# Kernel optimization log

Measured on AMD Instinct MI355X. Metric: run time of the kernel, lower is better.

Reference implementation:

```python
import jax, jax.numpy as jnp
import numpy as np

B, N, E, H = 32, 512, 256, 8
HD = E // H
EPS = 1e-5

def setup_inputs() -> dict:
    key = jax.random.key(0)
    ks = jax.random.split(key, 10)
    x = jax.random.normal(ks[0], (B, N, E), dtype=jnp.float32)
    # boolean masks: True = masked out. Keep diagonal unmasked so no row is fully masked.
    pre = jax.random.bernoulli(ks[1], 0.1, (B, H, N, N))
    eye = jnp.eye(N, dtype=bool)
    pre_mask = jnp.where(eye[None, None, :, :], False, pre)
    post_attn_mask = jax.random.bernoulli(ks[2], 0.1, (B, N))
    s = 1.0 / np.sqrt(E)
    in_proj_w = jax.random.uniform(ks[3], (3 * E, E), jnp.float32, -s, s)
    in_proj_b = jnp.zeros((3 * E,), jnp.float32)
    out_w = jax.random.uniform(ks[4], (E, E), jnp.float32, -s, s)
    out_b = jnp.zeros((E,), jnp.float32)
    gamma = jnp.ones((E,), jnp.float32)
    beta = jnp.zeros((E,), jnp.float32)
    return {"x": x, "pre_mask": pre_mask, "post_attn_mask": post_attn_mask,
            "in_proj_w": in_proj_w, "in_proj_b": in_proj_b,
            "out_w": out_w, "out_b": out_b, "gamma": gamma, "beta": beta}

def reference(x, pre_mask, post_attn_mask, in_proj_w, in_proj_b, out_w, out_b, gamma, beta):
    b, n, e = x.shape
    # fused qkv projection (matches nn.MultiheadAttention in_proj)
    qkv = x @ in_proj_w.T + in_proj_b            # [B,N,3E]
    q, k, v = jnp.split(qkv, 3, axis=-1)
    def heads(t):
        return t.reshape(b, n, H, HD).transpose(0, 2, 1, 3)  # [B,H,N,HD]
    q, k, v = heads(q), heads(k), heads(v)
    scores = jnp.einsum('bhqd,bhkd->bhqk', q * (HD ** -0.5), k)  # [B,H,N,N]
    scores = jnp.where(pre_mask, -1e9, scores)
    w = jax.nn.softmax(scores, axis=-1)                          # [B,H,N,N]
    o = jnp.einsum('bhqk,bhkd->bhqd', w, v)                      # [B,H,N,HD]
    o = o.transpose(0, 2, 1, 3).reshape(b, n, e)
    o = o @ out_w.T + out_b
    # post-attention mask: zero outputs of unavailable agents
    o = jnp.where(post_attn_mask[:, :, None], 0.0, o)
    # residual + LayerNorm
    y = x + o
    mu = y.mean(axis=-1, keepdims=True)
    var = y.var(axis=-1, keepdims=True)
    out = (y - mu) * jax.lax.rsqrt(var + EPS) * gamma + beta
    # attn_weights averaged over heads (PyTorch default average_attn_weights=True)
    attn_weights = w.mean(axis=1)                                # [B,N,N]
    return (out, attn_weights)
```

## Files before the change

kernel.cpp:

```cpp
#include <hip/hip_runtime.h>

#define BB 32
#define NN 512
#define EE 256
#define HH 8
#define HDD 32

typedef __attribute__((ext_vector_type(4))) float f32x4;
typedef __attribute__((ext_vector_type(8))) short s16x8;
typedef unsigned short ushort_t;
typedef unsigned int uint_t;

__device__ __forceinline__ ushort_t f2bf(float f) {
  union { float f; uint_t u; } v; v.f = f;
  uint_t r = v.u + 0x7fffu + ((v.u >> 16) & 1u);
  return (ushort_t)(r >> 16);
}
__device__ __forceinline__ uint_t pk2(float a, float b) {
  return (uint_t)f2bf(a) | ((uint_t)f2bf(b) << 16);
}
__device__ __forceinline__ float bf2f(ushort_t u) {
  union { uint_t u; float f; } v; v.u = ((uint_t)u) << 16;
  return v.f;
}

__global__ __launch_bounds__(256) void cvt_all(
    const float* __restrict__ x, const float* __restrict__ w1, const float* __restrict__ w2,
    ushort_t* __restrict__ xb, ushort_t* __restrict__ w1b, ushort_t* __restrict__ w2b) {
  const int NX = BB * NN * EE / 4;
  const int NW1 = 3 * EE * EE / 4;
  const int NW2 = EE * EE / 4;
  int i = blockIdx.x * 256 + threadIdx.x;
  const float* src; ushort_t* dst; int j;
  if (i < NX) { src = x; dst = xb; j = i; }
  else if (i < NX + NW1) { src = w1; dst = w1b; j = i - NX; }
  else if (i < NX + NW1 + NW2) { src = w2; dst = w2b; j = i - NX - NW1; }
  else return;
  float4 v = ((const float4*)src)[j];
  uint2 p; p.x = pk2(v.x, v.y); p.y = pk2(v.z, v.w);
  ((uint2*)dst)[j] = p;
}

__global__ __launch_bounds__(256) void qkv_mfma(
    const ushort_t* __restrict__ xb, const ushort_t* __restrict__ wb,
    const float* __restrict__ bias,
    ushort_t* __restrict__ Q, ushort_t* __restrict__ K, ushort_t* __restrict__ Vt) {
  __shared__ ushort_t sA[128][40];
  __shared__ ushort_t sB[128][40];
  int t = threadIdx.x;
  int bj = blockIdx.x % 6, bm = blockIdx.x / 6;
  int m0 = bm * 128, j0 = bj * 128;
  int w4 = t >> 6, lane = t & 63, quad = lane >> 4, l16 = lane & 15;
  int wy = w4 >> 1, wx = w4 & 1;
  f32x4 acc[4][4];
  #pragma unroll
  for (int a = 0; a < 4; a++)
    #pragma unroll
    for (int b = 0; b < 4; b++) acc[a][b] = (f32x4){0.f, 0.f, 0.f, 0.f};
  int sr2 = t >> 2, sc2 = (t & 3) * 8;
  for (int kk = 0; kk < 256; kk += 32) {
    __syncthreads();
    #pragma unroll
    for (int p = 0; p < 2; p++) {
      int r = sr2 + 64 * p;
      *(s16x8*)&sA[r][sc2] = *(const s16x8*)&xb[(size_t)(m0 + r) * 256 + kk + sc2];
      *(s16x8*)&sB[r][sc2] = *(const s16x8*)&wb[(size_t)(j0 + r) * 256 + kk + sc2];
    }
    __syncthreads();
    s16x8 af[4], bf[4];
    #pragma unroll
    for (int mt = 0; mt < 4; mt++)
      af[mt] = *(const s16x8*)&sA[wy * 64 + mt * 16 + l16][quad * 8];
    #pragma unroll
    for (int jt = 0; jt < 4; jt++)
      bf[jt] = *(const s16x8*)&sB[wx * 64 + jt * 16 + l16][quad * 8];
    #pragma unroll
    for (int mt = 0; mt < 4; mt++)
      #pragma unroll
      for (int jt = 0; jt < 4; jt++)
        acc[mt][jt] = __builtin_amdgcn_mfma_f32_16x16x32_bf16(af[mt], bf[jt], acc[mt][jt], 0, 0, 0);
  }
  #pragma unroll
  for (int jt = 0; jt < 4; jt++) {
    int j = j0 + wx * 64 + jt * 16 + l16;
    int which = j >> 8, e0 = j & 255, h = e0 >> 5, d0 = e0 & 31;
    float b = bias[j];
    #pragma unroll
    for (int mt = 0; mt < 4; mt++) {
      #pragma unroll
      for (int r = 0; r < 4; r++) {
        int m = m0 + wy * 64 + mt * 16 + quad * 4 + r;
        int bi = m >> 9, n = m & 511;
        ushort_t val = f2bf(acc[mt][jt][r] + b);
        if (which == 2) {
          Vt[((size_t)(bi * 8 + h) * 32 + d0) * 512 + n] = val;
        } else {
          ushort_t* dst = (which == 0) ? Q : K;
          dst[((size_t)(bi * 8 + h) * 512 + n) * 32 + d0] = val;
        }
      }
    }
  }
}

__global__ __launch_bounds__(256) void attn_fused(
    const ushort_t* __restrict__ Q, const ushort_t* __restrict__ K,
    const ushort_t* __restrict__ Vt, const int* __restrict__ pre_mask,
    const ushort_t* __restrict__ wob, const float* __restrict__ x,
    const float* __restrict__ out_b, const int* __restrict__ post_mask,
    const float* __restrict__ gamma, const float* __restrict__ beta,
    float* __restrict__ out, float* __restrict__ attnw) {
  __shared__ ushort_t sP[4][16 * 132];
  __shared__ float sSum[2][4][16];
  __shared__ float sO[4][16 * 33];
  __shared__ ushort_t sO16[16 * 260];
  __shared__ float sRed1[16][4];
  __shared__ float sRed2[16][4];

  int t = threadIdx.x;
  int bb = blockIdx.x >> 5;
  int q0 = (blockIdx.x & 31) << 4;
  int w = t >> 6, lane = t & 63, quad = lane >> 4, l16 = lane & 15;
  int kbase = w * 128;
  const float scale = 0.17677669529663687f;
  ushort_t* mysP = &sP[w][0];

  float wmean[4][8];
  #pragma unroll
  for (int i = 0; i < 4; i++)
    #pragma unroll
    for (int j = 0; j < 8; j++) wmean[i][j] = 0.f;

  for (int h = 0; h < 8; h++) {
    size_t base = ((size_t)(bb * 8 + h) * 512) * 32;
    const int* mbase = pre_mask + ((size_t)(bb * 8 + h) * 512 + q0) * 512;

    s16x8 afrag = *(const s16x8*)&Q[base + (size_t)(q0 + l16) * 32 + quad * 8];

    float psum[4] = {0.f, 0.f, 0.f, 0.f};
    #pragma unroll
    for (int t8 = 0; t8 < 8; t8++) {
      int n0 = kbase + t8 * 16;
      s16x8 bfrag = *(const s16x8*)&K[base + (size_t)(n0 + l16) * 32 + quad * 8];
      f32x4 acc = {0.f, 0.f, 0.f, 0.f};
      acc = __builtin_amdgcn_mfma_f32_16x16x32_bf16(afrag, bfrag, acc, 0, 0, 0);
      #pragma unroll
      for (int i = 0; i < 4; i++) {
        int msk = mbase[(quad * 4 + i) * 512 + n0 + l16];
        float e = msk ? 0.f : __expf(acc[i] * scale);
        mysP[(quad * 4 + i) * 132 + t8 * 16 + l16] = f2bf(e);
        psum[i] += e;
      }
    }
    #pragma unroll
    for (int i = 0; i < 4; i++) {
      float s = psum[i];
      s += __shfl_xor(s, 1, 64);
      s += __shfl_xor(s, 2, 64);
      s += __shfl_xor(s, 4, 64);
      s += __shfl_xor(s, 8, 64);
      psum[i] = s;
    }
    if (l16 == 0) {
      #pragma unroll
      for (int i = 0; i < 4; i++) sSum[h & 1][w][quad * 4 + i] = psum[i];
    }
    __syncthreads();

    float inv[4];
    #pragma unroll
    for (int i = 0; i < 4; i++) {
      int r = quad * 4 + i;
      inv[i] = 0.125f / (sSum[h & 1][0][r] + sSum[h & 1][1][r] + sSum[h & 1][2][r] + sSum[h & 1][3][r]);
    }
    #pragma unroll
    for (int t8 = 0; t8 < 8; t8++)
      #pragma unroll
      for (int i = 0; i < 4; i++)
        wmean[i][t8] += inv[i] * bf2f(mysP[(quad * 4 + i) * 132 + t8 * 16 + l16]);

    f32x4 oacc[2];
    oacc[0] = (f32x4){0.f, 0.f, 0.f, 0.f};
    oacc[1] = (f32x4){0.f, 0.f, 0.f, 0.f};
    #pragma unroll
    for (int ks = 0; ks < 4; ks++) {
      s16x8 pa = *(const s16x8*)&mysP[l16 * 132 + ks * 32 + quad * 8];
      #pragma unroll
      for (int dt = 0; dt < 2; dt++) {
        s16x8 vb = *(const s16x8*)&Vt[base + (size_t)(dt * 16 + l16) * 512 + kbase + ks * 32 + quad * 8];
        oacc[dt] = __builtin_amdgcn_mfma_f32_16x16x32_bf16(pa, vb, oacc[dt], 0, 0, 0);
      }
    }
    #pragma unroll
    for (int dt = 0; dt < 2; dt++)
      #pragma unroll
      for (int i = 0; i < 4; i++)
        sO[w][(quad * 4 + i) * 33 + dt * 16 + l16] = oacc[dt][i];
    __syncthreads();

    {
      int r = t >> 4;
      int c = (t & 15) * 2;
      float s0 = sO[0][r * 33 + c] + sO[1][r * 33 + c] + sO[2][r * 33 + c] + sO[3][r * 33 + c];
      float s1 = sO[0][r * 33 + c + 1] + sO[1][r * 33 + c + 1] + sO[2][r * 33 + c + 1] + sO[3][r * 33 + c + 1];
      float invr = 1.0f / (sSum[h & 1][0][r] + sSum[h & 1][1][r] + sSum[h & 1][2][r] + sSum[h & 1][3][r]);
      *(uint_t*)&sO16[r * 260 + h * 32 + c] = pk2(s0 * invr, s1 * invr);
    }
  }

  {
    float* arow = attnw + (size_t)(bb * 512 + q0) * 512;
    #pragma unroll
    for (int i = 0; i < 4; i++)
      #pragma unroll
      for (int t8 = 0; t8 < 8; t8++)
        arow[(quad * 4 + i) * 512 + kbase + t8 * 16 + l16] = wmean[i][t8];
  }
  __syncthreads();

  int jr0 = w * 64;
  f32x4 pacc[4];
  #pragma unroll
  for (int jt = 0; jt < 4; jt++) pacc[jt] = (f32x4){0.f, 0.f, 0.f, 0.f};
  #pragma unroll
  for (int kc = 0; kc < 8; kc++) {
    s16x8 pa = *(const s16x8*)&sO16[l16 * 260 + kc * 32 + quad * 8];
    #pragma unroll
    for (int jt = 0; jt < 4; jt++) {
      s16x8 bf = *(const s16x8*)&wob[(size_t)(jr0 + jt * 16 + l16) * 256 + kc * 32 + quad * 8];
      pacc[jt] = __builtin_amdgcn_mfma_f32_16x16x32_bf16(pa, bf, pacc[jt], 0, 0, 0);
    }
  }

  float g4[4], bt4[4], ob4[4];
  #pragma unroll
  for (int jt = 0; jt < 4; jt++) {
    int j = jr0 + jt * 16 + l16;
    g4[jt] = gamma[j]; bt4[jt] = beta[j]; ob4[jt] = out_b[j];
  }
  float yv[4][4];
  #pragma unroll
  for (int i = 0; i < 4; i++) {
    int r = quad * 4 + i;
    int m = bb * 512 + q0 + r;
    bool msk = post_mask[m] != 0;
    float s1 = 0.f, s2 = 0.f;
    #pragma unroll
    for (int jt = 0; jt < 4; jt++) {
      int j = jr0 + jt * 16 + l16;
      float p = msk ? 0.f : (pacc[jt][i] + ob4[jt]);
      float yy = x[(size_t)m * 256 + j] + p;
      yv[i][jt] = yy; s1 += yy; s2 += yy * yy;
    }
    s1 += __shfl_xor(s1, 1, 64); s1 += __shfl_xor(s1, 2, 64);
    s1 += __shfl_xor(s1, 4, 64); s1 += __shfl_xor(s1, 8, 64);
    s2 += __shfl_xor(s2, 1, 64); s2 += __shfl_xor(s2, 2, 64);
    s2 += __shfl_xor(s2, 4, 64); s2 += __shfl_xor(s2, 8, 64);
    if (l16 == 0) { sRed1[r][w] = s1; sRed2[r][w] = s2; }
  }
  __syncthreads();
  #pragma unroll
  for (int i = 0; i < 4; i++) {
    int r = quad * 4 + i;
    int m = bb * 512 + q0 + r;
    float S1 = sRed1[r][0] + sRed1[r][1] + sRed1[r][2] + sRed1[r][3];
    float S2 = sRed2[r][0] + sRed2[r][1] + sRed2[r][2] + sRed2[r][3];
    float mu = S1 * (1.0f / 256.0f);
    float var = S2 * (1.0f / 256.0f) - mu * mu;
    float rstd = rsqrtf(var + 1e-5f);
    #pragma unroll
    for (int jt = 0; jt < 4; jt++) {
      int j = jr0 + jt * 16 + l16;
      out[(size_t)m * 256 + j] = (yv[i][jt] - mu) * rstd * g4[jt] + bt4[jt];
    }
  }
}

extern "C" void kernel_launch(void* const* d_in, const int* in_sizes, int n_in,
                              void* d_out, int out_size, void* d_ws, size_t ws_size,
                              hipStream_t stream) {
  const float* x       = (const float*)d_in[0];
  const int*   pre_m   = (const int*)d_in[1];
  const int*   post_m  = (const int*)d_in[2];
  const float* in_w    = (const float*)d_in[3];
  const float* in_b    = (const float*)d_in[4];
  const float* out_w   = (const float*)d_in[5];
  const float* out_b   = (const float*)d_in[6];
  const float* gamma   = (const float*)d_in[7];
  const float* beta    = (const float*)d_in[8];
  float* out   = (float*)d_out;
  float* attnw = out + (size_t)BB * NN * EE;
  ushort_t* Q   = (ushort_t*)d_ws;
  ushort_t* K   = Q  + (size_t)BB * HH * NN * HDD;
  ushort_t* Vt  = K  + (size_t)BB * HH * NN * HDD;
  ushort_t* xb  = Vt + (size_t)BB * HH * NN * HDD;
  ushort_t* wib = xb + (size_t)BB * NN * EE;
  ushort_t* wob = wib + (size_t)3 * EE * EE;

  const int NCVT = BB * NN * EE / 4 + 3 * EE * EE / 4 + EE * EE / 4;
  cvt_all<<<dim3((NCVT + 255) / 256), dim3(256), 0, stream>>>(x, in_w, out_w, xb, wib, wob);
  qkv_mfma<<<dim3(768), dim3(256), 0, stream>>>(xb, wib, in_b, Q, K, Vt);
  attn_fused<<<dim3(1024), dim3(256), 0, stream>>>(Q, K, Vt, pre_m, wob, x, out_b, post_m,
                                                   gamma, beta, out, attnw);
}
```

Baseline: 456.5 us.

## Pack pre-mask into bitmask inside QKV GEMM and consume bits in attention

The QKV projection kernel now also reads the int32 pre_mask (256 MB) and compresses it into 64-bit ballot words, interleaving this streaming work with the GEMM k-loop. The attention kernel then reads the compact bitmask instead of the full int mask. It also accumulates head-averaged weights packed as bf16 pairs to cut registers and sets launch bounds for 4 blocks per CU. This adds bf16 rounding error to the averaged attention weights, and the full mask is still read once, now inside the GEMM kernel.

```diff
diff --git a/kernel.cpp b/kernel.cpp
--- a/kernel.cpp
+++ b/kernel.cpp
@@ -10,6 +10,7 @@
 typedef __attribute__((ext_vector_type(8))) short s16x8;
 typedef unsigned short ushort_t;
 typedef unsigned int uint_t;
+typedef unsigned long long ull_t;
 
 __device__ __forceinline__ ushort_t f2bf(float f) {
   union { float f; uint_t u; } v; v.f = f;
@@ -44,7 +45,8 @@
 __global__ __launch_bounds__(256) void qkv_mfma(
     const ushort_t* __restrict__ xb, const ushort_t* __restrict__ wb,
     const float* __restrict__ bias,
-    ushort_t* __restrict__ Q, ushort_t* __restrict__ K, ushort_t* __restrict__ Vt) {
+    ushort_t* __restrict__ Q, ushort_t* __restrict__ K, ushort_t* __restrict__ Vt,
+    const int* __restrict__ pre_mask, ull_t* __restrict__ mbits) {
   __shared__ ushort_t sA[128][40];
   __shared__ ushort_t sB[128][40];
   int t = threadIdx.x;
@@ -52,13 +54,15 @@
   int m0 = bm * 128, j0 = bj * 128;
   int w4 = t >> 6, lane = t & 63, quad = lane >> 4, l16 = lane & 15;
   int wy = w4 >> 1, wx = w4 & 1;
+  int wid = blockIdx.x * 4 + w4;
   f32x4 acc[4][4];
   #pragma unroll
   for (int a = 0; a < 4; a++)
     #pragma unroll
     for (int b = 0; b < 4; b++) acc[a][b] = (f32x4){0.f, 0.f, 0.f, 0.f};
   int sr2 = t >> 2, sc2 = (t & 3) * 8;
-  for (int kk = 0; kk < 256; kk += 32) {
+  for (int ks = 0; ks < 8; ks++) {
+    int kk = ks * 32;
     __syncthreads();
     #pragma unroll
     for (int p = 0; p < 2; p++) {
@@ -79,6 +83,15 @@
       #pragma unroll
       for (int jt = 0; jt < 4; jt++)
         acc[mt][jt] = __builtin_amdgcn_mfma_f32_16x16x32_bf16(af[mt], bf[jt], acc[mt][jt], 0, 0, 0);
+    #pragma unroll 4
+    for (int j = 0; j < 43; j++) {
+      int widx = (ks * 43 + j) * 3072 + wid;
+      if (widx < 1048576) {
+        int mv = pre_mask[(size_t)widx * 64 + lane];
+        ull_t bl = __ballot(mv != 0);
+        if (lane == 0) mbits[widx] = bl;
+      }
+    }
   }
   #pragma unroll
   for (int jt = 0; jt < 4; jt++) {
@@ -103,9 +116,9 @@
   }
 }
 
-__global__ __launch_bounds__(256) void attn_fused(
+__global__ __launch_bounds__(256, 4) void attn_fused(
     const ushort_t* __restrict__ Q, const ushort_t* __restrict__ K,
-    const ushort_t* __restrict__ Vt, const int* __restrict__ pre_mask,
+    const ushort_t* __restrict__ Vt, const uint_t* __restrict__ mbits32,
     const ushort_t* __restrict__ wob, const float* __restrict__ x,
     const float* __restrict__ out_b, const int* __restrict__ post_mask,
     const float* __restrict__ gamma, const float* __restrict__ beta,
@@ -125,17 +138,20 @@
   const float scale = 0.17677669529663687f;
   ushort_t* mysP = &sP[w][0];
 
-  float wmean[4][8];
-  #pragma unroll
-  for (int i = 0; i < 4; i++)
-    #pragma unroll
-    for (int j = 0; j < 8; j++) wmean[i][j] = 0.f;
+  uint_t wm[16];
+  #pragma unroll
+  for (int i = 0; i < 16; i++) wm[i] = 0u;
 
   for (int h = 0; h < 8; h++) {
     size_t base = ((size_t)(bb * 8 + h) * 512) * 32;
-    const int* mbase = pre_mask + ((size_t)(bb * 8 + h) * 512 + q0) * 512;
+    const uint_t* mb = mbits32 + ((size_t)(bb * 8 + h) * 512 + q0) * 16 + (kbase >> 5);
 
     s16x8 afrag = *(const s16x8*)&Q[base + (size_t)(q0 + l16) * 32 + quad * 8];
+
+    uint4 mrow[4];
+    #pragma unroll
+    for (int i = 0; i < 4; i++)
+      mrow[i] = *(const uint4*)&mb[(quad * 4 + i) * 16];
 
     float psum[4] = {0.f, 0.f, 0.f, 0.f};
     #pragma unroll
@@ -144,10 +160,11 @@
       s16x8 bfrag = *(const s16x8*)&K[base + (size_t)(n0 + l16) * 32 + quad * 8];
       f32x4 acc = {0.f, 0.f, 0.f, 0.f};
       acc = __builtin_amdgcn_mfma_f32_16x16x32_bf16(afrag, bfrag, acc, 0, 0, 0);
+      int sh = (t8 & 1) * 16 + l16;
       #pragma unroll
       for (int i = 0; i < 4; i++) {
-        int msk = mbase[(quad * 4 + i) * 512 + n0 + l16];
-        float e = msk ? 0.f : __expf(acc[i] * scale);
+        uint_t sel = ((const uint_t*)&mrow[i])[t8 >> 1];
+        float e = ((sel >> sh) & 1u) ? 0.f : __expf(acc[i] * scale);
         mysP[(quad * 4 + i) * 132 + t8 * 16 + l16] = f2bf(e);
         psum[i] += e;
       }
@@ -174,10 +191,16 @@
       inv[i] = 0.125f / (sSum[h & 1][0][r] + sSum[h & 1][1][r] + sSum[h & 1][2][r] + sSum[h & 1][3][r]);
     }
     #pragma unroll
-    for (int t8 = 0; t8 < 8; t8++)
-      #pragma unroll
-      for (int i = 0; i < 4; i++)
-        wmean[i][t8] += inv[i] * bf2f(mysP[(quad * 4 + i) * 132 + t8 * 16 + l16]);
+    for (int i = 0; i < 4; i++) {
+      #pragma unroll
+      for (int t4 = 0; t4 < 4; t4++) {
+        float a0 = inv[i] * bf2f(mysP[(quad * 4 + i) * 132 + (2 * t4) * 16 + l16]);
+        float a1 = inv[i] * bf2f(mysP[(quad * 4 + i) * 132 + (2 * t4 + 1) * 16 + l16]);
+        uint_t cur = wm[i * 4 + t4];
+        wm[i * 4 + t4] = pk2(bf2f((ushort_t)(cur & 0xffffu)) + a0,
+                             bf2f((ushort_t)(cur >> 16)) + a1);
+      }
+    }
 
     f32x4 oacc[2];
     oacc[0] = (f32x4){0.f, 0.f, 0.f, 0.f};
@@ -211,10 +234,14 @@
   {
     float* arow = attnw + (size_t)(bb * 512 + q0) * 512;
     #pragma unroll
-    for (int i = 0; i < 4; i++)
-      #pragma unroll
-      for (int t8 = 0; t8 < 8; t8++)
-        arow[(quad * 4 + i) * 512 + kbase + t8 * 16 + l16] = wmean[i][t8];
+    for (int i = 0; i < 4; i++) {
+      #pragma unroll
+      for (int t4 = 0; t4 < 4; t4++) {
+        uint_t c = wm[i * 4 + t4];
+        arow[(quad * 4 + i) * 512 + kbase + (2 * t4) * 16 + l16] = bf2f((ushort_t)(c & 0xffffu));
+        arow[(quad * 4 + i) * 512 + kbase + (2 * t4 + 1) * 16 + l16] = bf2f((ushort_t)(c >> 16));
+      }
+    }
   }
   __syncthreads();
 
@@ -296,10 +323,11 @@
   ushort_t* xb  = Vt + (size_t)BB * HH * NN * HDD;
   ushort_t* wib = xb + (size_t)BB * NN * EE;
   ushort_t* wob = wib + (size_t)3 * EE * EE;
+  ull_t* mbits  = (ull_t*)(wob + (size_t)EE * EE);
 
   const int NCVT = BB * NN * EE / 4 + 3 * EE * EE / 4 + EE * EE / 4;
   cvt_all<<<dim3((NCVT + 255) / 256), dim3(256), 0, stream>>>(x, in_w, out_w, xb, wib, wob);
-  qkv_mfma<<<dim3(768), dim3(256), 0, stream>>>(xb, wib, in_b, Q, K, Vt);
-  attn_fused<<<dim3(1024), dim3(256), 0, stream>>>(Q, K, Vt, pre_m, wob, x, out_b, post_m,
-                                                   gamma, beta, out, attnw);
-}
+  qkv_mfma<<<dim3(768), dim3(256), 0, stream>>>(xb, wib, in_b, Q, K, Vt, pre_m, mbits);
+  attn_fused<<<dim3(1024), dim3(256), 0, stream>>>(Q, K, Vt, (const uint_t*)mbits, wob, x,
+                                                   out_b, post_m, gamma, beta, out, attnw);
+}
```

Result: slower. 764.7 us (+67.5%).

## Prefetch mask into registers, pack head-mean accumulators as bf16, raise occupancy

Applied to the files above, without the earlier changes.

Loads all 32 pre-mask values for a head into registers before the QK MFMA loop, so the global mask loads are issued together and not interleaved with the exp computation. The head-averaged attention weight accumulators move from 32 fp32 registers to 16 packed bf16 pairs, and the launch bounds now request 4 blocks per CU to push occupancy up. The bf16 accumulation over 8 heads lowers the precision of attn_weights. The 32 extra mask registers work against the register saving and could force spills under the tighter occupancy bound.

```diff
diff --git a/kernel.cpp b/kernel.cpp
--- a/kernel.cpp
+++ b/kernel.cpp
@@ -103,7 +103,7 @@
   }
 }
 
-__global__ __launch_bounds__(256) void attn_fused(
+__global__ __launch_bounds__(256, 4) void attn_fused(
     const ushort_t* __restrict__ Q, const ushort_t* __restrict__ K,
     const ushort_t* __restrict__ Vt, const int* __restrict__ pre_mask,
     const ushort_t* __restrict__ wob, const float* __restrict__ x,
@@ -125,15 +125,20 @@
   const float scale = 0.17677669529663687f;
   ushort_t* mysP = &sP[w][0];
 
-  float wmean[4][8];
-  #pragma unroll
-  for (int i = 0; i < 4; i++)
-    #pragma unroll
-    for (int j = 0; j < 8; j++) wmean[i][j] = 0.f;
+  uint_t wm[16];
+  #pragma unroll
+  for (int i = 0; i < 16; i++) wm[i] = 0u;
 
   for (int h = 0; h < 8; h++) {
     size_t base = ((size_t)(bb * 8 + h) * 512) * 32;
     const int* mbase = pre_mask + ((size_t)(bb * 8 + h) * 512 + q0) * 512;
+
+    int mreg[32];
+    #pragma unroll
+    for (int t8 = 0; t8 < 8; t8++)
+      #pragma unroll
+      for (int i = 0; i < 4; i++)
+        mreg[t8 * 4 + i] = mbase[(quad * 4 + i) * 512 + kbase + t8 * 16 + l16];
 
     s16x8 afrag = *(const s16x8*)&Q[base + (size_t)(q0 + l16) * 32 + quad * 8];
 
@@ -146,8 +151,7 @@
       acc = __builtin_amdgcn_mfma_f32_16x16x32_bf16(afrag, bfrag, acc, 0, 0, 0);
       #pragma unroll
       for (int i = 0; i < 4; i++) {
-        int msk = mbase[(quad * 4 + i) * 512 + n0 + l16];
-        float e = msk ? 0.f : __expf(acc[i] * scale);
+        float e = mreg[t8 * 4 + i] ? 0.f : __expf(acc[i] * scale);
         mysP[(quad * 4 + i) * 132 + t8 * 16 + l16] = f2bf(e);
         psum[i] += e;
       }
@@ -174,10 +178,16 @@
       inv[i] = 0.125f / (sSum[h & 1][0][r] + sSum[h & 1][1][r] + sSum[h & 1][2][r] + sSum[h & 1][3][r]);
     }
     #pragma unroll
-    for (int t8 = 0; t8 < 8; t8++)
-      #pragma unroll
-      for (int i = 0; i < 4; i++)
-        wmean[i][t8] += inv[i] * bf2f(mysP[(quad * 4 + i) * 132 + t8 * 16 + l16]);
+    for (int i = 0; i < 4; i++) {
+      #pragma unroll
+      for (int t4 = 0; t4 < 4; t4++) {
+        float a0 = inv[i] * bf2f(mysP[(quad * 4 + i) * 132 + (2 * t4) * 16 + l16]);
+        float a1 = inv[i] * bf2f(mysP[(quad * 4 + i) * 132 + (2 * t4 + 1) * 16 + l16]);
+        uint_t cur = wm[i * 4 + t4];
+        wm[i * 4 + t4] = pk2(bf2f((ushort_t)(cur & 0xffffu)) + a0,
+                             bf2f((ushort_t)(cur >> 16)) + a1);
+      }
+    }
 
     f32x4 oacc[2];
     oacc[0] = (f32x4){0.f, 0.f, 0.f, 0.f};
@@ -211,10 +221,14 @@
   {
     float* arow = attnw + (size_t)(bb * 512 + q0) * 512;
     #pragma unroll
-    for (int i = 0; i < 4; i++)
-      #pragma unroll
-      for (int t8 = 0; t8 < 8; t8++)
-        arow[(quad * 4 + i) * 512 + kbase + t8 * 16 + l16] = wmean[i][t8];
+    for (int i = 0; i < 4; i++) {
+      #pragma unroll
+      for (int t4 = 0; t4 < 4; t4++) {
+        uint_t c = wm[i * 4 + t4];
+        arow[(quad * 4 + i) * 512 + kbase + (2 * t4) * 16 + l16] = bf2f((ushort_t)(c & 0xffffu));
+        arow[(quad * 4 + i) * 512 + kbase + (2 * t4 + 1) * 16 + l16] = bf2f((ushort_t)(c >> 16));
+      }
+    }
   }
   __syncthreads();
 
```

After: 461.5 us. About the same (+1.1%).
